# Kernel tuning notes

Hardware: AMD Instinct MI355X
Metric: run time of the kernel (lower is better)

## Reference

```python
import jax, jax.numpy as jnp
import numpy as np

SCALE_BASE = 512.0
GAMMA = 0.96875


def _xpos(x, downscale=False):
    # x: (b, l, hd). XPOS rotary with magnitude scaling (offset=0 path).
    b, l, hd = x.shape
    half = hd // 2
    pos = jnp.arange(l, dtype=jnp.float32)
    scale_vec = (jnp.arange(0, hd, 2, dtype=jnp.float32) + 0.4 * hd) / (1.4 * hd)  # (half,)
    scale = scale_vec[None, :] ** (pos / SCALE_BASE)[:, None]                      # (l, half)
    inv_freq = 1.0 / (10000.0 ** (jnp.arange(half, dtype=jnp.float32) / half))
    sinusoid = pos[:, None] * inv_freq[None, :]                                    # (l, half)
    sin, cos = jnp.sin(sinusoid), jnp.cos(sinusoid)
    if downscale:
        scale = 1.0 / scale
    # duplicate_interleave: each column repeated twice -> (l, hd)
    sin_s = jnp.repeat(sin * scale, 2, axis=-1)
    cos_s = jnp.repeat(cos * scale, 2, axis=-1)
    x1, x2 = x[..., ::2], x[..., 1::2]
    rot = jnp.stack((-x2, x1), axis=-1).reshape(x.shape)  # rotate_every_two
    return x * cos_s + rot * sin_s


def _get_D(l, gamma):
    n = jnp.arange(l)[:, None]
    m = jnp.arange(l)[None, :]
    diff = n - m
    # only compute gamma**diff where diff >= 0 to avoid inf/nan (torch zeroes NaNs)
    D = jnp.where(diff >= 0, gamma ** jnp.maximum(diff, 0).astype(jnp.float32), 0.0)
    return D


def setup_inputs() -> dict:
    key = jax.random.key(0)
    kx, kq, kk, kv = jax.random.split(key, 4)
    b, l, d, hd, vd = 4, 4096, 512, 64, 128
    X = jax.random.normal(kx, (b, l, d), dtype=jnp.float32)
    W_Q = jax.random.normal(kq, (d, hd), dtype=jnp.float32) / d
    W_K = jax.random.normal(kk, (d, hd), dtype=jnp.float32) / d
    W_V = jax.random.normal(kv, (d, vd), dtype=jnp.float32) / d
    return {"X": X, "W_Q": W_Q, "W_K": W_K, "W_V": W_V}


def reference(X, W_Q, W_K, W_V):
    l = X.shape[1]
    D = _get_D(l, GAMMA)                 # (l, l) lower-triangular decay
    Q = _xpos(X @ W_Q)                   # (b, l, hd)
    K = _xpos(X @ W_K, downscale=True)   # (b, l, hd)
    V = X @ W_V                          # (b, l, vd)
    ret = jnp.einsum('bnh,bmh->bnm', Q, K) * D[None]  # (b, l, l)
    # dropout omitted (deterministic reference / eval mode)
    return jnp.einsum('bnm,bmv->bnv', ret, V)
```

## Files before the change

kernel.cpp:

```cpp
#include <hip/hip_runtime.h>
#include <math.h>

#define B_ 4
#define L_ 4096
#define D_ 512
#define HD_ 64
#define VD_ 128
#define GAMMA_ 0.96875f
#define L2G_ (-0.045803595f)
#define GC_  (0.13108252f)
#define MAGIC_ 0x13572468u

typedef __attribute__((ext_vector_type(8))) short bf16x8;
typedef __attribute__((ext_vector_type(4))) float f32x4;
typedef unsigned short u16;
typedef unsigned int u32;

static __device__ __forceinline__ u16 f2b(float f) {
    u32 u = __float_as_uint(f);
    return (u16)((u + 0x7FFFu + ((u >> 16) & 1u)) >> 16);
}
static __device__ __forceinline__ float b2f(u16 h) {
    return __uint_as_float((u32)h << 16);
}
static __device__ __forceinline__ void store_b128_dev(u16* p, bf16x8 v) {
    asm volatile("global_store_dwordx4 %0, %1, off sc1" :: "v"(p), "v"(v) : "memory");
}

#define LDSFRAG(buf, rowblk, ks) \
    (*(const bf16x8*)&(buf)[((rowblk)*16 + ln15)*64 + \
        ((((ks)*4 + ln4) ^ ((((rowblk)*16 + ln15)) & 7)) << 3)])

__global__ __launch_bounds__(1024) void k_fused(
    const float* __restrict__ X,
    const float* __restrict__ WQ, const float* __restrict__ WK,
    const float* __restrict__ WV,
    u16* __restrict__ Pb, u32* __restrict__ flags, float* __restrict__ Out)
{
    __shared__ __align__(16) u16 ldsA[40960];
    __shared__ __align__(16) float4 Tl[2048];
    __shared__ __align__(16) u16 lds2[8192];

    const int tid  = threadIdx.x;
    const int lane = tid & 63;
    const int ln15 = lane & 15, ln4 = lane >> 4;
    const int wave = tid >> 6;
    const int raw  = blockIdx.x;
    const int g    = ((raw & 7) << 5) + (raw >> 3);
    const int t    = g & 63;
    const int row0 = g * 64;

    if (tid == 0)
        __hip_atomic_store(&flags[g], 0u, __ATOMIC_RELAXED, __HIP_MEMORY_SCOPE_AGENT);

    const int ar = tid >> 4, aq = tid & 15;
    const float* gA = X + (size_t)(row0 + ar)*D_ + aq*4;
    const int kg = tid >> 8, wn = tid & 255;
    const float* Wp; int ldw;
    if (wn < 64)       { Wp = WQ + wn;       ldw = 64;  }
    else if (wn < 128) { Wp = WK + (wn-64);  ldw = 64;  }
    else               { Wp = WV + (wn-128); ldw = 128; }

    float4 xb[2];
    float  wb[2][16];

    xb[0] = *(const float4*)gA;
    {
        const float* bp = Wp + (size_t)(kg*16) * ldw;
        #pragma unroll
        for (int j = 0; j < 16; ++j) wb[0][j] = bp[(size_t)j * ldw];
    }

    #pragma unroll
    for (int e0 = 0; e0 < 2; ++e0) {
        int e  = tid + (e0 << 10);
        int lr = e >> 5, ii = e & 31;
        float pos = (float)(((g & 63) << 6) + lr);
        float sv   = (2.0f*ii + 0.4f*HD_) * (1.0f/(1.4f*HD_));
        float sc   = exp2f(__log2f(sv) * pos * (1.0f/512.0f));
        float invf = exp2f((float)ii * (-13.287712379549449f/32.0f));
        float s, c; sincosf(pos * invf, &s, &c);
        Tl[e] = make_float4(c*sc, s*sc, c/sc, s/sc);
    }

    f32x4 acc[4] = {};

    #pragma unroll
    for (int kt = 0; kt < 8; ++kt) {
        const int cur = kt & 1, nxt = cur ^ 1;
        if (kt < 7) {
            xb[nxt] = *(const float4*)(gA + (kt+1)*64);
            const float* bp = Wp + (size_t)((kt+1)*64 + kg*16) * ldw;
            #pragma unroll
            for (int j = 0; j < 16; ++j) wb[nxt][j] = bp[(size_t)j * ldw];
        }
        u16* At = ldsA + cur*20480;
        u16* Bt = At + 4096;
        {
            ushort4 av = make_ushort4(f2b(xb[cur].x), f2b(xb[cur].y),
                                      f2b(xb[cur].z), f2b(xb[cur].w));
            *(ushort4*)&At[ar*64 + (((aq>>1) ^ (ar & 7)) << 3) + ((aq & 1) << 2)] = av;
            bf16x8 b0, b1;
            #pragma unroll
            for (int j = 0; j < 8; ++j) {
                b0[j] = (short)f2b(wb[cur][j]);
                b1[j] = (short)f2b(wb[cur][8+j]);
            }
            *(bf16x8*)&Bt[wn*64 + ((((kg<<1)  ) ^ (wn & 7)) << 3)] = b0;
            *(bf16x8*)&Bt[wn*64 + ((((kg<<1)+1) ^ (wn & 7)) << 3)] = b1;
        }
        __syncthreads();
        #pragma unroll
        for (int ks = 0; ks < 2; ++ks) {
            bf16x8 af[4], bfr;
            #pragma unroll
            for (int m = 0; m < 4; ++m) {
                int r = m*16 + ln15;
                af[m] = *(const bf16x8*)&At[r*64 + (((ks*4 + ln4) ^ (r & 7)) << 3)];
            }
            {
                int r = wave*16 + ln15;
                bfr = *(const bf16x8*)&Bt[r*64 + (((ks*4 + ln4) ^ (r & 7)) << 3)];
            }
            #pragma unroll
            for (int m = 0; m < 4; ++m)
                acc[m] = __builtin_amdgcn_mfma_f32_16x16x32_bf16(af[m], bfr, acc[m], 0, 0, 0);
        }
    }

    u16* Qs   = ldsA;
    u16* Ks_  = ldsA + 4096;
    u16* Kd_l = ldsA + 8192;
    u16* Vt_l = ldsA + 12288;
    u16* As   = Kd_l;
    u16* Pb_l = lds2;
    u16* Ss   = lds2;

    const int mode = wave >> 2;
    const int col  = wave*16 + ln15;
    #pragma unroll
    for (int m = 0; m < 4; ++m) {
        const int j0 = m*16 + (ln4 << 2);
        const int cj = j0 >> 3;
        u16 pk[4];
        #pragma unroll
        for (int r = 0; r < 4; ++r) {
            int jrow = j0 + r;
            float v = acc[m][r];
            float p = __shfl_xor(v, 1, 64);
            if (mode < 2) {
                int h = col & 63;
                float4 tt = Tl[jrow*32 + (h >> 1)];
                float c = (mode == 0) ? tt.x : tt.z;
                float s = (mode == 0) ? tt.y : tt.w;
                float o = ((h & 1) == 0) ? (v*c - p*s) : (v*c + p*s);
                u16 ob = f2b(o);
                int swz = jrow*64 + (((h >> 3) ^ (jrow & 7)) << 3) + (h & 7);
                if (mode == 0) Qs[swz] = ob;
                else {
                    Ks_[swz] = ob;
                    pk[r] = f2b(o * exp2f((float)(63 - jrow) * L2G_));
                }
            } else {
                pk[r] = f2b(v);
            }
        }
        if (mode == 1) {
            int h = col & 63;
            *(ushort4*)&Kd_l[h*64 + ((cj ^ (h & 7)) << 3) + (j0 & 7)] =
                make_ushort4(pk[0], pk[1], pk[2], pk[3]);
        } else if (mode >= 2) {
            int v = col - 128;
            *(ushort4*)&Vt_l[v*64 + ((cj ^ (v & 7)) << 3) + (j0 & 7)] =
                make_ushort4(pk[0], pk[1], pk[2], pk[3]);
        }
    }
    __syncthreads();

    {
        f32x4 accp[2] = {};
        const int vr = wave >> 1, hcb = (wave & 1) * 2;
        #pragma unroll
        for (int ks = 0; ks < 2; ++ks) {
            int rv = vr*16 + ln15;
            bf16x8 av = *(const bf16x8*)&Vt_l[rv*64 + (((ks*4 + ln4) ^ (rv & 7)) << 3)];
            #pragma unroll
            for (int e = 0; e < 2; ++e) {
                int rh = (hcb + e)*16 + ln15;
                bf16x8 bk = *(const bf16x8*)&Kd_l[rh*64 + (((ks*4 + ln4) ^ (rh & 7)) << 3)];
                accp[e] = __builtin_amdgcn_mfma_f32_16x16x32_bf16(av, bk, accp[e], 0, 0, 0);
            }
        }
        #pragma unroll
        for (int e = 0; e < 2; ++e)
            #pragma unroll
            for (int r = 0; r < 4; ++r) {
                int v = vr*16 + (ln4 << 2) + r;
                int h = (hcb + e)*16 + ln15;
                Pb_l[v*64 + h] = f2b(accp[e][r]);
            }
    }
    __syncthreads();
    store_b128_dev(&Pb[(size_t)g*8192 + tid*8], *(const bf16x8*)&Pb_l[tid*8]);
    asm volatile("s_waitcnt vmcnt(0)" ::: "memory");
    __syncthreads();
    if (tid == 0)
        __hip_atomic_store(&flags[g], MAGIC_, __ATOMIC_RELAXED, __HIP_MEMORY_SCOPE_AGENT);

    const int nwin = (t < 16) ? t : 16;
    if (tid < nwin) {
        int it = 0;
        while (__hip_atomic_load(&flags[g - 1 - tid], __ATOMIC_RELAXED,
                                 __HIP_MEMORY_SCOPE_AGENT) != MAGIC_ && it < (1 << 20)) {
            __builtin_amdgcn_s_sleep(2);
            ++it;
        }
    }
    __syncthreads();

    {
        int v = tid >> 3, h0 = (tid & 7) * 8;
        float accs[8] = {};
        const u16* pb = Pb + (size_t)(g - 1)*8192 + v*64 + h0;
        float w = 1.0f;
        #pragma unroll 8
        for (int s = 0; s < nwin; ++s) {
            bf16x8 p0 = *(const bf16x8*)(pb - (size_t)s*8192);
            #pragma unroll
            for (int e = 0; e < 8; ++e)
                accs[e] = fmaf(w, b2f((u16)p0[e]), accs[e]);
            w *= GC_;
        }
        bf16x8 s0;
        #pragma unroll
        for (int e = 0; e < 8; ++e) s0[e] = (short)f2b(accs[e]);
        *(bf16x8*)&Ss[v*64 + (((h0 >> 3) ^ (v & 7)) << 3)] = s0;
    }

    const int fr  = wave & 3;
    const int fc  = wave >> 2;
    const int vcb = (wave >> 2) * 2;

    f32x4 sacc = {};
    #pragma unroll
    for (int ks = 0; ks < 2; ++ks)
        sacc = __builtin_amdgcn_mfma_f32_16x16x32_bf16(
            LDSFRAG(Qs, fr, ks), LDSFRAG(Ks_, fc, ks), sacc, 0, 0, 0);
    #pragma unroll
    for (int r = 0; r < 4; ++r) {
        int i = fr*16 + (ln4 << 2) + r;
        int j = fc*16 + ln15;
        float a = (j <= i) ? sacc[r] * exp2f((float)(i - j) * L2G_) : 0.0f;
        As[i*64 + (((j >> 3) ^ (i & 7)) << 3) + (j & 7)] = f2b(a);
    }
    __syncthreads();

    f32x4 oacc[2] = {};
    #pragma unroll
    for (int ks = 0; ks < 2; ++ks) {
        bf16x8 aq2 = LDSFRAG(Qs, fr, ks);
        #pragma unroll
        for (int n = 0; n < 2; ++n)
            oacc[n] = __builtin_amdgcn_mfma_f32_16x16x32_bf16(aq2, LDSFRAG(Ss, vcb+n, ks), oacc[n], 0, 0, 0);
    }
    #pragma unroll
    for (int r = 0; r < 4; ++r) {
        float gsc = exp2f((float)(fr*16 + (ln4 << 2) + r + 1) * L2G_);
        oacc[0][r] *= gsc; oacc[1][r] *= gsc;
    }
    #pragma unroll
    for (int ks = 0; ks < 2; ++ks) {
        bf16x8 aa = LDSFRAG(As, fr, ks);
        #pragma unroll
        for (int n = 0; n < 2; ++n)
            oacc[n] = __builtin_amdgcn_mfma_f32_16x16x32_bf16(aa, LDSFRAG(Vt_l, vcb+n, ks), oacc[n], 0, 0, 0);
    }
    #pragma unroll
    for (int n = 0; n < 2; ++n)
        #pragma unroll
        for (int r = 0; r < 4; ++r) {
            int i = fr*16 + (ln4 << 2) + r;
            int v = (vcb+n)*16 + ln15;
            Out[(size_t)(row0 + i)*VD_ + v] = oacc[n][r];
        }
}

extern "C" void kernel_launch(void* const* d_in, const int* in_sizes, int n_in,
                              void* d_out, int out_size, void* d_ws, size_t ws_size,
                              hipStream_t stream)
{
    const float* X  = (const float*)d_in[0];
    const float* WQ = (const float*)d_in[1];
    const float* WK = (const float*)d_in[2];
    const float* WV = (const float*)d_in[3];
    float* out = (float*)d_out;

    u16* Pb    = (u16*)d_ws;
    u32* flags = (u32*)(Pb + 2097152);

    k_fused<<<256, 1024, 0, stream>>>(X, WQ, WK, WV, Pb, flags, out);
}
```

Before: 27.90 us.

## Vectorize weight loads and retile projection MFMA to 2x2 wave tiles

Weight matrices are now loaded as row-contiguous float4 vectors (four columns by four k-rows per thread) instead of sixteen strided scalar loads down a column. The result is transposed into bf16 LDS with ushort4 stores. The projection GEMM's wave tiling changes from each wave owning a 64x16 strip (four A fragments, one B) to a 32x32 tile (two A, two B). This reduces LDS fragment reads per MFMA, and the rotary/decay epilogue is reindexed to match. The intent is to cut global load instruction count and LDS traffic in the fused projection prologue, at the cost of more complex epilogue indexing.

```diff
diff --git a/kernel.cpp b/kernel.cpp
--- a/kernel.cpp
+++ b/kernel.cpp
@@ -55,21 +55,21 @@
 
     const int ar = tid >> 4, aq = tid & 15;
     const float* gA = X + (size_t)(row0 + ar)*D_ + aq*4;
-    const int kg = tid >> 8, wn = tid & 255;
-    const float* Wp; int ldw;
-    if (wn < 64)       { Wp = WQ + wn;       ldw = 64;  }
-    else if (wn < 128) { Wp = WK + (wn-64);  ldw = 64;  }
-    else               { Wp = WV + (wn-128); ldw = 128; }
+    const int kq = tid >> 6, nq = tid & 63;
+    const int n4 = nq << 2;
+    const float* Mp; int ldw, c0;
+    if (n4 < 64)       { Mp = WQ; ldw = 64;  c0 = n4; }
+    else if (n4 < 128) { Mp = WK; ldw = 64;  c0 = n4 - 64; }
+    else               { Mp = WV; ldw = 128; c0 = n4 - 128; }
+    const int cg = kq >> 1, klo = (kq & 1) << 2;
 
     float4 xb[2];
-    float  wb[2][16];
+    f32x4  wr[2][4];
 
     xb[0] = *(const float4*)gA;
-    {
-        const float* bp = Wp + (size_t)(kg*16) * ldw;
-        #pragma unroll
-        for (int j = 0; j < 16; ++j) wb[0][j] = bp[(size_t)j * ldw];
-    }
+    #pragma unroll
+    for (int j = 0; j < 4; ++j)
+        wr[0][j] = *(const f32x4*)(Mp + (size_t)(kq*4 + j)*ldw + c0);
 
     #pragma unroll
     for (int e0 = 0; e0 < 2; ++e0) {
@@ -83,16 +83,18 @@
         Tl[e] = make_float4(c*sc, s*sc, c/sc, s/sc);
     }
 
-    f32x4 acc[4] = {};
+    const int mb2 = wave >> 3;
+    const int nb2 = wave & 7;
+    f32x4 acc[2][2] = {};
 
     #pragma unroll
     for (int kt = 0; kt < 8; ++kt) {
         const int cur = kt & 1, nxt = cur ^ 1;
         if (kt < 7) {
             xb[nxt] = *(const float4*)(gA + (kt+1)*64);
-            const float* bp = Wp + (size_t)((kt+1)*64 + kg*16) * ldw;
-            #pragma unroll
-            for (int j = 0; j < 16; ++j) wb[nxt][j] = bp[(size_t)j * ldw];
+            #pragma unroll
+            for (int j = 0; j < 4; ++j)
+                wr[nxt][j] = *(const f32x4*)(Mp + (size_t)((kt+1)*64 + kq*4 + j)*ldw + c0);
         }
         u16* At = ldsA + cur*20480;
         u16* Bt = At + 4096;
@@ -100,31 +102,33 @@
             ushort4 av = make_ushort4(f2b(xb[cur].x), f2b(xb[cur].y),
                                       f2b(xb[cur].z), f2b(xb[cur].w));
             *(ushort4*)&At[ar*64 + (((aq>>1) ^ (ar & 7)) << 3) + ((aq & 1) << 2)] = av;
-            bf16x8 b0, b1;
-            #pragma unroll
-            for (int j = 0; j < 8; ++j) {
-                b0[j] = (short)f2b(wb[cur][j]);
-                b1[j] = (short)f2b(wb[cur][8+j]);
-            }
-            *(bf16x8*)&Bt[wn*64 + ((((kg<<1)  ) ^ (wn & 7)) << 3)] = b0;
-            *(bf16x8*)&Bt[wn*64 + ((((kg<<1)+1) ^ (wn & 7)) << 3)] = b1;
+            #pragma unroll
+            for (int i = 0; i < 4; ++i) {
+                int wn = n4 + i;
+                ushort4 bvv = make_ushort4(f2b(wr[cur][0][i]), f2b(wr[cur][1][i]),
+                                           f2b(wr[cur][2][i]), f2b(wr[cur][3][i]));
+                *(ushort4*)&Bt[wn*64 + ((cg ^ (wn & 7)) << 3) + klo] = bvv;
+            }
         }
         __syncthreads();
         #pragma unroll
         for (int ks = 0; ks < 2; ++ks) {
-            bf16x8 af[4], bfr;
-            #pragma unroll
-            for (int m = 0; m < 4; ++m) {
-                int r = m*16 + ln15;
+            bf16x8 af[2], bfr[2];
+            #pragma unroll
+            for (int m = 0; m < 2; ++m) {
+                int r = (mb2*2 + m)*16 + ln15;
                 af[m] = *(const bf16x8*)&At[r*64 + (((ks*4 + ln4) ^ (r & 7)) << 3)];
             }
-            {
-                int r = wave*16 + ln15;
-                bfr = *(const bf16x8*)&Bt[r*64 + (((ks*4 + ln4) ^ (r & 7)) << 3)];
-            }
-            #pragma unroll
-            for (int m = 0; m < 4; ++m)
-                acc[m] = __builtin_amdgcn_mfma_f32_16x16x32_bf16(af[m], bfr, acc[m], 0, 0, 0);
+            #pragma unroll
+            for (int n = 0; n < 2; ++n) {
+                int r = (nb2*2 + n)*16 + ln15;
+                bfr[n] = *(const bf16x8*)&Bt[r*64 + (((ks*4 + ln4) ^ (r & 7)) << 3)];
+            }
+            #pragma unroll
+            for (int m = 0; m < 2; ++m)
+                #pragma unroll
+                for (int n = 0; n < 2; ++n)
+                    acc[m][n] = __builtin_amdgcn_mfma_f32_16x16x32_bf16(af[m], bfr[n], acc[m][n], 0, 0, 0);
         }
     }
 
@@ -136,43 +140,46 @@
     u16* Pb_l = lds2;
     u16* Ss   = lds2;
 
-    const int mode = wave >> 2;
-    const int col  = wave*16 + ln15;
-    #pragma unroll
-    for (int m = 0; m < 4; ++m) {
-        const int j0 = m*16 + (ln4 << 2);
+    const int mode = (nb2 < 2) ? 0 : (nb2 < 4) ? 1 : 2;
+    #pragma unroll
+    for (int m = 0; m < 2; ++m) {
+        const int j0 = (mb2*2 + m)*16 + (ln4 << 2);
         const int cj = j0 >> 3;
-        u16 pk[4];
-        #pragma unroll
-        for (int r = 0; r < 4; ++r) {
-            int jrow = j0 + r;
-            float v = acc[m][r];
-            float p = __shfl_xor(v, 1, 64);
-            if (mode < 2) {
+        #pragma unroll
+        for (int n = 0; n < 2; ++n) {
+            const int col = nb2*32 + n*16 + ln15;
+            u16 pk[4];
+            #pragma unroll
+            for (int r = 0; r < 4; ++r) {
+                int jrow = j0 + r;
+                float v = acc[m][n][r];
+                float p = __shfl_xor(v, 1, 64);
+                if (mode < 2) {
+                    int h = col & 63;
+                    float4 tt = Tl[jrow*32 + (h >> 1)];
+                    float c = (mode == 0) ? tt.x : tt.z;
+                    float s = (mode == 0) ? tt.y : tt.w;
+                    float o = ((h & 1) == 0) ? (v*c - p*s) : (v*c + p*s);
+                    u16 ob = f2b(o);
+                    int swz = jrow*64 + (((h >> 3) ^ (jrow & 7)) << 3) + (h & 7);
+                    if (mode == 0) Qs[swz] = ob;
+                    else {
+                        Ks_[swz] = ob;
+                        pk[r] = f2b(o * exp2f((float)(63 - jrow) * L2G_));
+                    }
+                } else {
+                    pk[r] = f2b(v);
+                }
+            }
+            if (mode == 1) {
                 int h = col & 63;
-                float4 tt = Tl[jrow*32 + (h >> 1)];
-                float c = (mode == 0) ? tt.x : tt.z;
-                float s = (mode == 0) ? tt.y : tt.w;
-                float o = ((h & 1) == 0) ? (v*c - p*s) : (v*c + p*s);
-                u16 ob = f2b(o);
-                int swz = jrow*64 + (((h >> 3) ^ (jrow & 7)) << 3) + (h & 7);
-                if (mode == 0) Qs[swz] = ob;
-                else {
-                    Ks_[swz] = ob;
-                    pk[r] = f2b(o * exp2f((float)(63 - jrow) * L2G_));
-                }
-            } else {
-                pk[r] = f2b(v);
-            }
-        }
-        if (mode == 1) {
-            int h = col & 63;
-            *(ushort4*)&Kd_l[h*64 + ((cj ^ (h & 7)) << 3) + (j0 & 7)] =
-                make_ushort4(pk[0], pk[1], pk[2], pk[3]);
-        } else if (mode >= 2) {
-            int v = col - 128;
-            *(ushort4*)&Vt_l[v*64 + ((cj ^ (v & 7)) << 3) + (j0 & 7)] =
-                make_ushort4(pk[0], pk[1], pk[2], pk[3]);
+                *(ushort4*)&Kd_l[h*64 + ((cj ^ (h & 7)) << 3) + (j0 & 7)] =
+                    make_ushort4(pk[0], pk[1], pk[2], pk[3]);
+            } else if (mode == 2) {
+                int v = col - 128;
+                *(ushort4*)&Vt_l[v*64 + ((cj ^ (v & 7)) << 3) + (j0 & 7)] =
+                    make_ushort4(pk[0], pk[1], pk[2], pk[3]);
+            }
         }
     }
     __syncthreads();
```

Measured after the change: 29.79 us. 6.8% more time.
